# Kernel optimization log

Hardware: AMD Instinct MI355X
Metric: run time of the kernel (lower is better)

Reference implementation:

```python
import jax, jax.numpy as jnp
import numpy as np

D_MODEL = 2048
N_HEADS = 16
D_HEAD = D_MODEL // N_HEADS
FF = 4 * D_MODEL
B, L = 2, 2048


def setup_inputs() -> dict:
    key = jax.random.key(0)
    ks = jax.random.split(key, 12)
    s = 0.02
    inp = {
        "x": jax.random.normal(ks[0], (B, L, D_MODEL), jnp.float32),
        "rope_cos": jnp.cos(jnp.arange(L)[:, None] / (10000.0 ** (jnp.arange(D_HEAD) / D_HEAD))).astype(jnp.float32),
        "rope_sin": jnp.sin(jnp.arange(L)[:, None] / (10000.0 ** (jnp.arange(D_HEAD) / D_HEAD))).astype(jnp.float32),
        "mask": jnp.ones((B, L), jnp.int32),
        "w_norm1": jnp.ones((D_MODEL,), jnp.float32),
        "w_norm2": jnp.ones((D_MODEL,), jnp.float32),
        # linear weights stored as [in, out] (transposed torch layout)
        "wq": jax.random.normal(ks[1], (D_MODEL, D_MODEL), jnp.float32) * s,
        "wk": jax.random.normal(ks[2], (D_MODEL, D_MODEL), jnp.float32) * s,
        "wv": jax.random.normal(ks[3], (D_MODEL, D_MODEL), jnp.float32) * s,
        "wo": jax.random.normal(ks[4], (D_MODEL, D_MODEL), jnp.float32) * s,
        "w_ff1": jax.random.normal(ks[5], (D_MODEL, FF), jnp.float32) * s,
        "w_ff2": jax.random.normal(ks[6], (FF, D_MODEL), jnp.float32) * s,
    }
    return inp


def _rmsnorm(x, w):
    eps = jnp.finfo(x.dtype).eps
    return x * jax.lax.rsqrt(jnp.mean(x * x, axis=-1, keepdims=True) + eps) * w


def _rotate_half(x):
    x1, x2 = jnp.split(x, 2, axis=-1)
    return jnp.concatenate([-x2, x1], axis=-1)


def reference(x, rope_cos, rope_sin, mask, w_norm1, w_norm2, wq, wk, wv, wo, w_ff1, w_ff2):
    b, l, d = x.shape
    h, dh = N_HEADS, D_HEAD

    residual = x
    xn = _rmsnorm(x, w_norm1)
    # project and split heads: [B, H, L, DH]
    q = (xn @ wq).reshape(b, l, h, dh).transpose(0, 2, 1, 3)
    k = (xn @ wk).reshape(b, l, h, dh).transpose(0, 2, 1, 3)
    v = (xn @ wv).reshape(b, l, h, dh).transpose(0, 2, 1, 3)

    cos = rope_cos[None, None]  # [1,1,L,DH]
    sin = rope_sin[None, None]
    q = q * cos + _rotate_half(q) * sin
    k = k * cos + _rotate_half(k) * sin

    scores = jnp.einsum("bhqd,bhkd->bhqk", q, k) * (dh ** -0.5)
    causal = jnp.tril(jnp.ones((l, l), bool))  # allowed positions
    allowed = causal[None, None] & (mask[:, None, None, :] != 0)
    scores = jnp.where(allowed, scores, -jnp.inf)
    attn = jax.nn.softmax(scores, axis=-1)  # dropout is identity in eval

    out = jnp.einsum("bhqk,bhkd->bhqd", attn, v)
    out = out.transpose(0, 2, 1, 3).reshape(b, l, d)
    x = residual + out @ wo

    xn2 = _rmsnorm(x, w_norm2)
    ff = jax.nn.silu(xn2 @ w_ff1) @ w_ff2
    return x + ff
```

## Files before the change

### kernel.cpp

```cpp
#include <hip/hip_runtime.h>


typedef __bf16 bf16;
typedef __bf16 bf16x8 __attribute__((ext_vector_type(8)));
typedef float  f32x4  __attribute__((ext_vector_type(4)));

__device__ __forceinline__ void gload16(const void* g, void* l) {
  __builtin_amdgcn_global_load_lds((const __attribute__((address_space(1))) void*)g,
                                   (__attribute__((address_space(3))) void*)l,
                                   16, 0, 0);
}

#define CBAR asm volatile("" ::: "memory")
#define WAITV(N) asm volatile("s_waitcnt vmcnt(" #N ")" ::: "memory")
#define LGKM0 asm volatile("s_waitcnt lgkmcnt(0)" ::: "memory")
#define BARR { CBAR; __builtin_amdgcn_s_barrier(); CBAR; }

__global__ __launch_bounds__(256) void rmsnorm_to_bf16(
    const float* __restrict__ x, const float* __restrict__ w, bf16* __restrict__ out)
{
  const int D = 2048;
  const int row = blockIdx.x;
  const int tid = threadIdx.x;
  const float* xr = x + (size_t)row * D;
  float4 a = ((const float4*)xr)[tid * 2];
  float4 c = ((const float4*)xr)[tid * 2 + 1];
  float ss = a.x*a.x + a.y*a.y + a.z*a.z + a.w*a.w
           + c.x*c.x + c.y*c.y + c.z*c.z + c.w*c.w;
  #pragma unroll
  for (int m = 1; m < 64; m <<= 1) ss += __shfl_xor(ss, m, 64);
  __shared__ float red[4];
  if ((tid & 63) == 0) red[tid >> 6] = ss;
  __syncthreads();
  float tot = red[0] + red[1] + red[2] + red[3];
  float rms = rsqrtf(tot * (1.0f / D) + 1.1920929e-7f);
  const float* wr = w + tid * 8;
  float vals[8] = {a.x, a.y, a.z, a.w, c.x, c.y, c.z, c.w};
  bf16x8 o;
  #pragma unroll
  for (int j = 0; j < 8; ++j) o[j] = (bf16)(vals[j] * rms * wr[j]);
  *(bf16x8*)(out + (size_t)row * D + tid * 8) = o;
}

__global__ __launch_bounds__(256) void transpose_to_bf16(
    const float* __restrict__ in, bf16* __restrict__ out, int R, int C)
{
  __shared__ float tile[32][33];
  const int tx = threadIdx.x, ty = threadIdx.y;
  const int c0 = blockIdx.x * 32, r0 = blockIdx.y * 32;
  #pragma unroll
  for (int i = 0; i < 4; ++i)
    tile[ty + i * 8][tx] = in[(size_t)(r0 + ty + i * 8) * C + c0 + tx];
  __syncthreads();
  #pragma unroll
  for (int i = 0; i < 4; ++i)
    out[(size_t)(c0 + ty + i * 8) * R + r0 + tx] = (bf16)tile[tx][ty + i * 8];
}

__global__ __launch_bounds__(256) void v_transpose(
    const bf16* __restrict__ v, bf16* __restrict__ vt)
{
  const int L = 2048, DM = 2048;
  __shared__ bf16 tile[32][33];
  const int tx = threadIdx.x, ty = threadIdx.y;
  const int k0 = blockIdx.x * 32;
  const int d0 = blockIdx.y * 32;
  const int bh = blockIdx.z;
  const int b = bh >> 4, h = bh & 15;
  #pragma unroll
  for (int i = 0; i < 4; ++i)
    tile[ty + i * 8][tx] = v[(size_t)(b * L + k0 + ty + i * 8) * DM + h * 128 + d0 + tx];
  __syncthreads();
  #pragma unroll
  for (int i = 0; i < 4; ++i) {
    const int d = d0 + ty + i * 8;
    const int key = k0 + tx;
    const int keysw = (key & ~63) | (((((key >> 3) & 7) ^ (d & 7)) << 3)) | (key & 7);
    vt[(size_t)(bh * 128 + d) * L + keysw] = tile[tx][ty + i * 8];
  }
}

template<int EPI>
__global__ __launch_bounds__(512, 2) void gemm256(
    const bf16* __restrict__ A, const bf16* __restrict__ Bt,
    void* Cout, const float* __restrict__ resid, int M, int N, int K)
{
  __shared__ bf16 sA[2][2][128 * 64];
  __shared__ bf16 sB[2][2][128 * 64];

  const int tid = threadIdx.x, lane = tid & 63, w = tid >> 6;
  const int wm = w >> 2, wn = w & 3;
  const int lo = lane & 15, hi = lane >> 4;
  const int lo7 = lo & 7;

  const int nbn = N >> 8;
  const int nwg = gridDim.x;
  int swz = blockIdx.x;
  if ((nwg & 7) == 0) { const int cpx = nwg >> 3; swz = (swz & 7) * cpx + (swz >> 3); }
  const int bm = swz / nbn, bn = swz % nbn;

  const int r0 = tid >> 3,         s0 = (tid & 7) ^ (r0 & 7);
  const int r1 = (512 + tid) >> 3, s1 = ((512 + tid) & 7) ^ (r1 & 7);
  const bf16* Ab = A  + (size_t)(bm * 256) * K;
  const bf16* Bb = Bt + (size_t)(bn * 256) * K;
  const size_t o0 = (size_t)r0 * K + s0 * 8;
  const size_t o1 = (size_t)r1 * K + s1 * 8;
  const int dst0 = (w * 64) * 8, dst1 = (512 + w * 64) * 8;
  const size_t rhK = (size_t)128 * K;

  bf16x8 afA[2][4], b0[2][2], b1[2][2];
  f32x4 acc[8][4] = {};
  const int NT = K >> 6;

  auto stageA = [&](int b, int rh, int kt) {
    const bf16* s = Ab + rh * rhK + (size_t)kt * 64;
    gload16(s + o0, &sA[b][rh][dst0]);
    gload16(s + o1, &sA[b][rh][dst1]);
  };
  auto stageB = [&](int b, int rh, int kt) {
    const bf16* s = Bb + rh * rhK + (size_t)kt * 64;
    gload16(s + o0, &sB[b][rh][dst0]);
    gload16(s + o1, &sB[b][rh][dst1]);
  };
  auto loadA = [&](int b, int rh) {
    #pragma unroll
    for (int ks = 0; ks < 2; ++ks)
      #pragma unroll
      for (int m = 0; m < 4; ++m) {
        const int row = wm * 64 + m * 16 + lo;
        afA[ks][m] = *(const bf16x8*)&sA[b][rh][row * 64 + (((ks * 4 + hi) ^ lo7) << 3)];
      }
  };
  auto loadB = [&](bf16x8 (&d)[2][2], int b, int rh) {
    #pragma unroll
    for (int ks = 0; ks < 2; ++ks)
      #pragma unroll
      for (int nj = 0; nj < 2; ++nj) {
        const int row = wn * 32 + nj * 16 + lo;
        d[ks][nj] = *(const bf16x8*)&sB[b][rh][row * 64 + (((ks * 4 + hi) ^ lo7) << 3)];
      }
  };
  auto mfma16 = [&](bf16x8 (&bf)[2][2], int mb, int nb2) {
    __builtin_amdgcn_s_setprio(1);
    #pragma unroll
    for (int ks = 0; ks < 2; ++ks)
      #pragma unroll
      for (int m = 0; m < 4; ++m)
        #pragma unroll
        for (int nj = 0; nj < 2; ++nj)
          acc[mb + m][nb2 + nj] = __builtin_amdgcn_mfma_f32_16x16x32_bf16(
              afA[ks][m], bf[ks][nj], acc[mb + m][nb2 + nj], 0, 0, 0);
    __builtin_amdgcn_s_setprio(0);
  };

  stageA(0, 0, 0); stageB(0, 0, 0); stageB(0, 1, 0); stageA(0, 1, 0);
  WAITV(4);
  BARR;

  for (int t = 0; t < NT; ++t) {
    const int buf = t & 1, nb = buf ^ 1;
    const bool st = (t + 1 < NT);
    loadA(buf, 0);
    loadB(b0, buf, 0);
    if (st) stageA(nb, 0, t + 1);
    BARR; LGKM0;
    mfma16(b0, 0, 0);
    if (st) { WAITV(4); } else { WAITV(0); }
    BARR;
    loadB(b1, buf, 1);
    if (st) stageB(nb, 0, t + 1);
    BARR; LGKM0;
    mfma16(b1, 0, 2);
    if (st) { WAITV(4); }
    BARR;
    loadA(buf, 1);
    if (st) stageB(nb, 1, t + 1);
    BARR; LGKM0;
    mfma16(b1, 4, 2);
    BARR;
    if (st) stageA(nb, 1, t + 1);
    BARR; LGKM0;
    mfma16(b0, 4, 0);
    if (st) { WAITV(4); }
    BARR;
  }

  #pragma unroll
  for (int mi = 0; mi < 8; ++mi) {
    #pragma unroll
    for (int j = 0; j < 4; ++j) {
      const size_t row = (size_t)(bm * 256 + (mi >> 2) * 128 + wm * 64 + (mi & 3) * 16 + hi * 4 + j);
      #pragma unroll
      for (int ni = 0; ni < 4; ++ni) {
        const int col = bn * 256 + (ni >> 1) * 128 + wn * 32 + (ni & 1) * 16 + lo;
        const float v = acc[mi][ni][j];
        if constexpr (EPI == 2) {
          ((bf16*)Cout)[row * (size_t)N + col] = (bf16)(v / (1.0f + __expf(-v)));
        } else {
          ((bf16*)Cout)[(size_t)(col >> 11) * 8388608 + row * 2048 + (col & 2047)] = (bf16)v;
        }
      }
    }
  }
}

__global__ __launch_bounds__(512, 1) void gemm128(
    const bf16* __restrict__ A, const bf16* __restrict__ Bt,
    float* __restrict__ Cout, const float* __restrict__ resid, int M, int N, int K)
{
  __shared__ bf16 sA[2][128 * 64];
  __shared__ bf16 sB[2][2][128 * 64];

  const int tid = threadIdx.x, lane = tid & 63, w = tid >> 6;
  const int wm = w >> 2, wn = w & 3;
  const int lo = lane & 15, hi = lane >> 4;
  const int lo7 = lo & 7;

  const int nbn = N >> 8;
  const int nwg = gridDim.x;
  int swz = blockIdx.x;
  if ((nwg & 7) == 0) { const int cpx = nwg >> 3; swz = (swz & 7) * cpx + (swz >> 3); }
  const int bm = swz / nbn, bn = swz % nbn;

  const int r0 = tid >> 3,         s0 = (tid & 7) ^ (r0 & 7);
  const int r1 = (512 + tid) >> 3, s1 = ((512 + tid) & 7) ^ (r1 & 7);
  const bf16* Ab = A  + (size_t)(bm * 128) * K;
  const bf16* Bb = Bt + (size_t)(bn * 256) * K;
  const size_t o0 = (size_t)r0 * K + s0 * 8;
  const size_t o1 = (size_t)r1 * K + s1 * 8;
  const int dst0 = (w * 64) * 8, dst1 = (512 + w * 64) * 8;
  const size_t nhK = (size_t)128 * K;

  bf16x8 afA[2][4], b0[2][2], b1[2][2];
  f32x4 acc[4][4] = {};
  const int NT = K >> 6;

  auto stageA = [&](int b, int kt) {
    const bf16* s = Ab + (size_t)kt * 64;
    gload16(s + o0, &sA[b][dst0]);
    gload16(s + o1, &sA[b][dst1]);
  };
  auto stageB = [&](int b, int nh, int kt) {
    const bf16* s = Bb + nh * nhK + (size_t)kt * 64;
    gload16(s + o0, &sB[b][nh][dst0]);
    gload16(s + o1, &sB[b][nh][dst1]);
  };
  auto loadA = [&](int b) {
    #pragma unroll
    for (int ks = 0; ks < 2; ++ks)
      #pragma unroll
      for (int m = 0; m < 4; ++m) {
        const int row = wm * 64 + m * 16 + lo;
        afA[ks][m] = *(const bf16x8*)&sA[b][row * 64 + (((ks * 4 + hi) ^ lo7) << 3)];
      }
  };
  auto loadB = [&](bf16x8 (&d)[2][2], int b, int nh) {
    #pragma unroll
    for (int ks = 0; ks < 2; ++ks)
      #pragma unroll
      for (int nj = 0; nj < 2; ++nj) {
        const int row = wn * 32 + nj * 16 + lo;
        d[ks][nj] = *(const bf16x8*)&sB[b][nh][row * 64 + (((ks * 4 + hi) ^ lo7) << 3)];
      }
  };
  auto mfma16 = [&](bf16x8 (&bf)[2][2], int nb2) {
    __builtin_amdgcn_s_setprio(1);
    #pragma unroll
    for (int ks = 0; ks < 2; ++ks)
      #pragma unroll
      for (int m = 0; m < 4; ++m)
        #pragma unroll
        for (int nj = 0; nj < 2; ++nj)
          acc[m][nb2 + nj] = __builtin_amdgcn_mfma_f32_16x16x32_bf16(
              afA[ks][m], bf[ks][nj], acc[m][nb2 + nj], 0, 0, 0);
    __builtin_amdgcn_s_setprio(0);
  };

  stageA(0, 0); stageB(0, 0, 0); stageB(0, 1, 0);
  WAITV(0);
  BARR;

  for (int t = 0; t < NT; ++t) {
    const int buf = t & 1, nb = buf ^ 1;
    const bool st = (t + 1 < NT);
    loadA(buf);
    loadB(b0, buf, 0);
    if (st) stageA(nb, t + 1);
    BARR; LGKM0;
    mfma16(b0, 0);
    if (st) { WAITV(2); } else { WAITV(0); }
    BARR;
    loadB(b1, buf, 1);
    if (st) { stageB(nb, 0, t + 1); stageB(nb, 1, t + 1); }
    BARR; LGKM0;
    mfma16(b1, 2);
    if (st) { WAITV(2); }
    BARR;
  }

  #pragma unroll
  for (int mi = 0; mi < 4; ++mi) {
    #pragma unroll
    for (int j = 0; j < 4; ++j) {
      const size_t row = (size_t)(bm * 128 + wm * 64 + mi * 16 + hi * 4 + j);
      const size_t ro = row * (size_t)N;
      #pragma unroll
      for (int ni = 0; ni < 4; ++ni) {
        const int col = bn * 256 + (ni >> 1) * 128 + wn * 32 + (ni & 1) * 16 + lo;
        Cout[ro + col] = acc[mi][ni][j] + resid[ro + col];
      }
    }
  }
}

__global__ __launch_bounds__(256) void rope_qk(
    bf16* q, const bf16* __restrict__ k, bf16* __restrict__ kswz,
    const float* __restrict__ cs, const float* __restrict__ sn)
{
  const int L = 2048, DM = 2048;
  const int idx = blockIdx.x * 256 + threadIdx.x;
  const int m = idx >> 7;
  const int rem = idx & 127;
  const int h = rem >> 3, t8 = rem & 7;
  const int pos = m & (L - 1);
  const int d0 = t8 * 8;
  const float* cb = cs + (size_t)pos * 128 + d0;
  const float* sb = sn + (size_t)pos * 128 + d0;
  float4 c1a = *(const float4*)(cb);      float4 c1b = *(const float4*)(cb + 4);
  float4 c2a = *(const float4*)(cb + 64); float4 c2b = *(const float4*)(cb + 68);
  float4 s1a = *(const float4*)(sb);      float4 s1b = *(const float4*)(sb + 4);
  float4 s2a = *(const float4*)(sb + 64); float4 s2b = *(const float4*)(sb + 68);
  float c1[8] = {c1a.x,c1a.y,c1a.z,c1a.w,c1b.x,c1b.y,c1b.z,c1b.w};
  float c2[8] = {c2a.x,c2a.y,c2a.z,c2a.w,c2b.x,c2b.y,c2b.z,c2b.w};
  float s1[8] = {s1a.x,s1a.y,s1a.z,s1a.w,s1b.x,s1b.y,s1b.z,s1b.w};
  float s2[8] = {s2a.x,s2a.y,s2a.z,s2a.w,s2b.x,s2b.y,s2b.z,s2b.w};
  const size_t base = (size_t)m * DM + h * 128 + d0;

  {
    bf16x8 x1 = *(bf16x8*)(q + base);
    bf16x8 x2 = *(bf16x8*)(q + base + 64);
    bf16x8 o1, o2;
    #pragma unroll
    for (int j = 0; j < 8; ++j) {
      const float a = (float)x1[j], b = (float)x2[j];
      o1[j] = (bf16)(a * c1[j] - b * s1[j]);
      o2[j] = (bf16)(b * c2[j] + a * s2[j]);
    }
    *(bf16x8*)(q + base) = o1;
    *(bf16x8*)(q + base + 64) = o2;
  }
  {
    bf16x8 x1 = *(const bf16x8*)(k + base);
    bf16x8 x2 = *(const bf16x8*)(k + base + 64);
    bf16x8 o1, o2;
    #pragma unroll
    for (int j = 0; j < 8; ++j) {
      const float a = (float)x1[j], b = (float)x2[j];
      o1[j] = (bf16)(a * c1[j] - b * s1[j]);
      o2[j] = (bf16)(b * c2[j] + a * s2[j]);
    }
    const int s = pos & 15;
    const int p1 = t8 ^ s;
    const int p2 = (8 + t8) ^ s;
    bf16* kr = kswz + (size_t)m * DM + h * 128;
    *(bf16x8*)(kr + p1 * 8) = o1;
    *(bf16x8*)(kr + p2 * 8) = o2;
  }
}

__global__ __launch_bounds__(256, 2) void attn_fwd(
    const bf16* __restrict__ Q, const bf16* __restrict__ Kswz,
    const bf16* __restrict__ VT, const int* __restrict__ mask,
    bf16* __restrict__ O)
{
  const int L = 2048, DM = 2048;
  __shared__ bf16 Kt[2][64 * 128];
  __shared__ bf16 Vt[2][128 * 64];
  __shared__ bf16 Plds[4][16 * 64];

  const int tid = threadIdx.x, lane = tid & 63, w = tid >> 6;
  const int lo = lane & 15, hi = lane >> 4;
  const int s7 = lo & 7;
  const int n = blockIdx.x;
  const int xcd = n & 7, slot = n >> 3;
  const int bh = xcd + 8 * (slot >> 5);
  const int tile = 31 - (slot & 31);
  const int b = bh >> 4, h = bh & 15;
  const int qrow = tile * 64 + w * 16;
  const float scale = 0.08838834764831845f;
  const float NEG_INF = -__builtin_inff();

  bf16x8 qf[4];
  {
    const bf16* qb = Q + (size_t)(b * L + qrow + lo) * DM + h * 128;
    #pragma unroll
    for (int ds = 0; ds < 4; ++ds) qf[ds] = *(const bf16x8*)(qb + ds * 32 + hi * 8);
  }

  float mrow[4] = {NEG_INF, NEG_INF, NEG_INF, NEG_INF};
  float lrow[4] = {0.f, 0.f, 0.f, 0.f};
  f32x4 oacc[8] = {};

  const bf16* vsrc[4];
  const bf16* ksrc[4];
  #pragma unroll
  for (int i = 0; i < 4; ++i) {
    const int gv = i * 256 + tid;
    vsrc[i] = VT + (size_t)(bh * 128 + (gv >> 3)) * L + (gv & 7) * 8;
    const int gk = i * 256 + tid;
    ksrc[i] = Kswz + (size_t)(b * L + (gk >> 4)) * DM + h * 128 + (gk & 15) * 8;
  }

  #pragma unroll
  for (int i = 0; i < 4; ++i) {
    gload16(ksrc[i], &Kt[0][(i * 256 + w * 64) * 8]);
    gload16(vsrc[i], &Vt[0][(i * 256 + w * 64) * 8]);
  }
  __syncthreads();

  const int nkt = tile + 1;
  for (int kt = 0; kt < nkt; ++kt) {
    const int buf = kt & 1;
    if (kt + 1 < nkt) {
      #pragma unroll
      for (int i = 0; i < 4; ++i) {
        gload16(ksrc[i] + (size_t)(kt + 1) * 64 * DM, &Kt[buf ^ 1][(i * 256 + w * 64) * 8]);
        gload16(vsrc[i] + (kt + 1) * 64,              &Vt[buf ^ 1][(i * 256 + w * 64) * 8]);
      }
    }

    int mk[4];
    #pragma unroll
    for (int kb = 0; kb < 4; ++kb) mk[kb] = mask[b * L + kt * 64 + kb * 16 + lo];

    f32x4 S[4];
    __builtin_amdgcn_s_setprio(1);
    #pragma unroll
    for (int kb = 0; kb < 4; ++kb) {
      f32x4 s = {};
      #pragma unroll
      for (int ds = 0; ds < 4; ++ds) {
        const bf16x8 kf = *(const bf16x8*)&Kt[buf][(kb * 16 + lo) * 128 + (((ds * 4 + hi) ^ lo) * 8)];
        s = __builtin_amdgcn_mfma_f32_16x16x32_bf16(qf[ds], kf, s, 0, 0, 0);
      }
      S[kb] = s;
    }
    __builtin_amdgcn_s_setprio(0);

    #pragma unroll
    for (int kb = 0; kb < 4; ++kb) {
      const int kidx = kt * 64 + kb * 16 + lo;
      #pragma unroll
      for (int j = 0; j < 4; ++j) {
        const float sv = S[kb][j] * scale;
        S[kb][j] = (mk[kb] != 0 && kidx <= qrow + hi * 4 + j) ? sv : NEG_INF;
      }
    }

    float p[4][4];
    #pragma unroll
    for (int j = 0; j < 4; ++j) {
      float tm = fmaxf(fmaxf(S[0][j], S[1][j]), fmaxf(S[2][j], S[3][j]));
      tm = fmaxf(tm, __shfl_xor(tm, 1, 64));
      tm = fmaxf(tm, __shfl_xor(tm, 2, 64));
      tm = fmaxf(tm, __shfl_xor(tm, 4, 64));
      tm = fmaxf(tm, __shfl_xor(tm, 8, 64));
      const float mn = fmaxf(mrow[j], tm);
      const float mn2 = (mn == NEG_INF) ? 0.f : mn;
      const float alpha = __expf(mrow[j] - mn2);
      float ps = 0.f;
      #pragma unroll
      for (int kb = 0; kb < 4; ++kb) { p[kb][j] = __expf(S[kb][j] - mn2); ps += p[kb][j]; }
      ps += __shfl_xor(ps, 1, 64);
      ps += __shfl_xor(ps, 2, 64);
      ps += __shfl_xor(ps, 4, 64);
      ps += __shfl_xor(ps, 8, 64);
      lrow[j] = lrow[j] * alpha + ps;
      mrow[j] = mn;
      #pragma unroll
      for (int n2 = 0; n2 < 8; ++n2) oacc[n2][j] *= alpha;
    }

    #pragma unroll
    for (int kb = 0; kb < 4; ++kb)
      #pragma unroll
      for (int j = 0; j < 4; ++j) {
        const int row = hi * 4 + j;
        Plds[w][row * 64 + ((((kb * 2 + (lo >> 3)) ^ (row & 7))) << 3) + (lo & 7)] = (bf16)p[kb][j];
      }

    __builtin_amdgcn_s_setprio(1);
    #pragma unroll
    for (int ks = 0; ks < 2; ++ks) {
      const bf16x8 pa = *(const bf16x8*)&Plds[w][lo * 64 + (((ks * 4 + hi) ^ s7) << 3)];
      #pragma unroll
      for (int n2 = 0; n2 < 8; ++n2) {
        const int r = n2 * 16 + lo;
        const bf16x8 vf = *(const bf16x8*)&Vt[buf][r * 64 + (((ks * 4 + hi) ^ s7) << 3)];
        oacc[n2] = __builtin_amdgcn_mfma_f32_16x16x32_bf16(pa, vf, oacc[n2], 0, 0, 0);
      }
    }
    __builtin_amdgcn_s_setprio(0);

    __syncthreads();
  }

  float inv[4];
  #pragma unroll
  for (int j = 0; j < 4; ++j) inv[j] = (lrow[j] > 0.f) ? 1.f / lrow[j] : 0.f;
  bf16* ob = O + (size_t)(b * L + qrow) * DM + h * 128;
  #pragma unroll
  for (int n2 = 0; n2 < 8; ++n2)
    #pragma unroll
    for (int j = 0; j < 4; ++j)
      ob[(size_t)(hi * 4 + j) * DM + n2 * 16 + lo] = (bf16)(oacc[n2][j] * inv[j]);
}

extern "C" void kernel_launch(void* const* d_in, const int* in_sizes, int n_in,
                              void* d_out, int out_size, void* d_ws, size_t ws_size,
                              hipStream_t stream)
{
  (void)in_sizes; (void)n_in; (void)out_size; (void)ws_size;
  const float* x        = (const float*)d_in[0];
  const float* rope_cos = (const float*)d_in[1];
  const float* rope_sin = (const float*)d_in[2];
  const int*   mask     = (const int*)d_in[3];
  const float* w_norm1  = (const float*)d_in[4];
  const float* w_norm2  = (const float*)d_in[5];
  const float* wq       = (const float*)d_in[6];
  const float* wk       = (const float*)d_in[7];
  const float* wv       = (const float*)d_in[8];
  const float* wo       = (const float*)d_in[9];
  const float* w_ff1    = (const float*)d_in[10];
  const float* w_ff2    = (const float*)d_in[11];
  float* out = (float*)d_out;

  const int M = 4096, D = 2048, FFD = 8192;
  char* ws = (char*)d_ws;
  const size_t WSLAB = 8388608ull;
  const size_t XNB   = 16777216ull;
  bf16* wqt  = (bf16*)(ws);
  bf16* wkt  = (bf16*)(ws + WSLAB);
  bf16* wvt  = (bf16*)(ws + 2 * WSLAB);
  bf16* wot  = (bf16*)(ws + 3 * WSLAB);
  char* pool = ws + 4 * WSLAB;
  bf16* xn   = (bf16*)(pool);
  bf16* qb   = (bf16*)(pool + XNB);
  bf16* kb   = (bf16*)(pool + 2 * XNB);
  bf16* vb   = (bf16*)(pool + 3 * XNB);
  bf16* ao   = (bf16*)(pool + 4 * XNB);
  bf16* vt   = (bf16*)(pool);
  bf16* kswz = (bf16*)(pool + 3 * XNB);
  bf16* ff1t = (bf16*)(ws);
  bf16* hmid = (bf16*)(pool);
  bf16* ff2t = (bf16*)(ws);
  bf16* xn2  = (bf16*)(pool + 4 * XNB);

  const dim3 tb(32, 8);

  rmsnorm_to_bf16<<<M, 256, 0, stream>>>(x, w_norm1, xn);
  transpose_to_bf16<<<dim3(D / 32, D / 32), tb, 0, stream>>>(wq, wqt, D, D);
  transpose_to_bf16<<<dim3(D / 32, D / 32), tb, 0, stream>>>(wk, wkt, D, D);
  transpose_to_bf16<<<dim3(D / 32, D / 32), tb, 0, stream>>>(wv, wvt, D, D);
  transpose_to_bf16<<<dim3(D / 32, D / 32), tb, 0, stream>>>(wo, wot, D, D);

  gemm256<3><<<(M / 256) * (6144 / 256), 512, 0, stream>>>(xn, wqt, qb, nullptr, M, 6144, D);

  v_transpose<<<dim3(2048 / 32, 128 / 32, 32), tb, 0, stream>>>(vb, vt);

  rope_qk<<<2048, 256, 0, stream>>>(qb, kb, kswz, rope_cos, rope_sin);

  attn_fwd<<<1024, 256, 0, stream>>>(qb, kswz, vt, mask, ao);

  gemm128<<<(M / 128) * (D / 256), 512, 0, stream>>>(ao, wot, out, x, M, D, D);

  rmsnorm_to_bf16<<<M, 256, 0, stream>>>(out, w_norm2, xn2);

  transpose_to_bf16<<<dim3(FFD / 32, D / 32), tb, 0, stream>>>(w_ff1, ff1t, D, FFD);
  gemm256<2><<<(M / 256) * (FFD / 256), 512, 0, stream>>>(xn2, ff1t, hmid, nullptr, M, FFD, D);

  transpose_to_bf16<<<dim3(D / 32, FFD / 32), tb, 0, stream>>>(w_ff2, ff2t, FFD, D);
  gemm128<<<(M / 128) * (D / 256), 512, 0, stream>>>(hmid, ff2t, out, out, M, D, FFD);
}
```

Baseline: 674.3 us.

## Double-buffer GEMM register fragments and prefetch next tile to cut barriers

Reworks the gemm256 main loop to keep two sets of A and B fragments in registers. The next k-tile's first A/B fragments are read from LDS at the end of the current iteration, and the separate barrier plus lgkmcnt wait before each MFMA group is dropped, so LDS reads overlap with MFMA work. vmcnt waits are tightened to match the new staging order. Launch bounds go from 2 to 1 waves-per-EU target, which gives room for the extra fragment registers. The 128KB of shared memory per block already limits residency to one block. The risk is higher register pressure and subtler ordering correctness across buffers.

```diff
diff --git a/kernel.cpp b/kernel.cpp
--- a/kernel.cpp
+++ b/kernel.cpp
@@ -81,7 +81,7 @@
 }
 
 template<int EPI>
-__global__ __launch_bounds__(512, 2) void gemm256(
+__global__ __launch_bounds__(512, 1) void gemm256(
     const bf16* __restrict__ A, const bf16* __restrict__ Bt,
     void* Cout, const float* __restrict__ resid, int M, int N, int K)
 {
@@ -108,7 +108,7 @@
   const int dst0 = (w * 64) * 8, dst1 = (512 + w * 64) * 8;
   const size_t rhK = (size_t)128 * K;
 
-  bf16x8 afA[2][4], b0[2][2], b1[2][2];
+  bf16x8 a0[2][4], a1[2][4], b0[2][2], b1[2][2];
   f32x4 acc[8][4] = {};
   const int NT = K >> 6;
 
@@ -122,13 +122,13 @@
     gload16(s + o0, &sB[b][rh][dst0]);
     gload16(s + o1, &sB[b][rh][dst1]);
   };
-  auto loadA = [&](int b, int rh) {
+  auto loadA = [&](bf16x8 (&d)[2][4], int b, int rh) {
     #pragma unroll
     for (int ks = 0; ks < 2; ++ks)
       #pragma unroll
       for (int m = 0; m < 4; ++m) {
         const int row = wm * 64 + m * 16 + lo;
-        afA[ks][m] = *(const bf16x8*)&sA[b][rh][row * 64 + (((ks * 4 + hi) ^ lo7) << 3)];
+        d[ks][m] = *(const bf16x8*)&sA[b][rh][row * 64 + (((ks * 4 + hi) ^ lo7) << 3)];
       }
   };
   auto loadB = [&](bf16x8 (&d)[2][2], int b, int rh) {
@@ -140,7 +140,7 @@
         d[ks][nj] = *(const bf16x8*)&sB[b][rh][row * 64 + (((ks * 4 + hi) ^ lo7) << 3)];
       }
   };
-  auto mfma16 = [&](bf16x8 (&bf)[2][2], int mb, int nb2) {
+  auto mfma16 = [&](bf16x8 (&a)[2][4], bf16x8 (&bf)[2][2], int mb, int nb2) {
     __builtin_amdgcn_s_setprio(1);
     #pragma unroll
     for (int ks = 0; ks < 2; ++ks)
@@ -149,39 +149,39 @@
         #pragma unroll
         for (int nj = 0; nj < 2; ++nj)
           acc[mb + m][nb2 + nj] = __builtin_amdgcn_mfma_f32_16x16x32_bf16(
-              afA[ks][m], bf[ks][nj], acc[mb + m][nb2 + nj], 0, 0, 0);
+              a[ks][m], bf[ks][nj], acc[mb + m][nb2 + nj], 0, 0, 0);
     __builtin_amdgcn_s_setprio(0);
   };
 
   stageA(0, 0, 0); stageB(0, 0, 0); stageB(0, 1, 0); stageA(0, 1, 0);
-  WAITV(4);
+  WAITV(0);
   BARR;
+  loadA(a0, 0, 0);
+  loadB(b0, 0, 0);
 
   for (int t = 0; t < NT; ++t) {
     const int buf = t & 1, nb = buf ^ 1;
     const bool st = (t + 1 < NT);
-    loadA(buf, 0);
-    loadB(b0, buf, 0);
+    loadB(b1, buf, 1);
     if (st) stageA(nb, 0, t + 1);
-    BARR; LGKM0;
-    mfma16(b0, 0, 0);
-    if (st) { WAITV(4); } else { WAITV(0); }
+    mfma16(a0, b0, 0, 0);
+    if (st) { WAITV(2); } else { WAITV(0); }
     BARR;
-    loadB(b1, buf, 1);
+    loadA(a1, buf, 1);
     if (st) stageB(nb, 0, t + 1);
-    BARR; LGKM0;
-    mfma16(b1, 0, 2);
-    if (st) { WAITV(4); }
+    mfma16(a0, b1, 0, 2);
     BARR;
-    loadA(buf, 1);
     if (st) stageB(nb, 1, t + 1);
-    BARR; LGKM0;
-    mfma16(b1, 4, 2);
+    mfma16(a1, b1, 4, 2);
+    if (st) { WAITV(2); }
     BARR;
-    if (st) stageA(nb, 1, t + 1);
-    BARR; LGKM0;
-    mfma16(b0, 4, 0);
-    if (st) { WAITV(4); }
+    mfma16(a1, b0, 4, 0);
+    if (st) {
+      loadA(a0, nb, 0);
+      loadB(b0, nb, 0);
+      stageA(nb, 1, t + 1);
+      WAITV(2);
+    }
     BARR;
   }
 
```

Measured after the change: 663.3 us. About the same (-1.6%).
